# Kernel optimization log

Hardware: AMD Instinct MI355X
Metric: run time of the kernel (lower is better)

## Reference

```python
import jax, jax.numpy as jnp
import numpy as np

N_NODES = 50000
N_EDGES = 160000
D = 512
N_GRAPHS = 64
EPS = 1e-5


def setup_inputs() -> dict:
    key = jax.random.key(0)
    ks = jax.random.split(key, 8)
    node = jax.random.normal(ks[0], (N_NODES, D), dtype=jnp.float32)
    edge_index = jax.random.randint(ks[1], (2, N_EDGES), 0, N_NODES, dtype=jnp.int64)
    edge_attr = jax.random.uniform(ks[2], (N_EDGES,), dtype=jnp.float32)
    batch_ptr = jnp.sort(jax.random.randint(ks[3], (N_NODES,), 0, N_GRAPHS, dtype=jnp.int64))
    W = jax.random.normal(ks[4], (D, D), dtype=jnp.float32) / np.float32(np.sqrt(D))
    b = jnp.zeros((D,), dtype=jnp.float32)
    gn_weight = jnp.ones((D,), dtype=jnp.float32)
    gn_bias = jnp.zeros((D,), dtype=jnp.float32)
    gn_mean_scale = jnp.ones((D,), dtype=jnp.float32)
    return {"node": node, "edge_attr": edge_attr, "W": W, "b": b,
            "gn_weight": gn_weight, "gn_bias": gn_bias, "gn_mean_scale": gn_mean_scale,
            "edge_index": edge_index, "batch_ptr": batch_ptr}


def _gcn_conv(x, edge_index, edge_weight, W, b):
    # x: [N, D]. PyG GCNConv(normalize=True): lin -> add self-loops -> D^-1/2 A D^-1/2 -> + bias
    x = x @ W  # [N, D]
    loop = jnp.arange(N_NODES, dtype=edge_index.dtype)
    row = jnp.concatenate([edge_index[0], loop])  # source
    col = jnp.concatenate([edge_index[1], loop])  # target
    w = jnp.concatenate([edge_weight, jnp.ones((N_NODES,), dtype=x.dtype)])
    deg = jax.ops.segment_sum(w, col, num_segments=N_NODES)  # weighted in-degree incl. self-loop
    dis = jnp.where(deg > 0, jax.lax.rsqrt(deg), 0.0)
    norm = dis[row] * w * dis[col]  # [E+N]
    msgs = x[row] * norm[:, None]  # gather + scale
    out = jax.ops.segment_sum(msgs, col, num_segments=N_NODES)  # scatter-add
    return out + b


def _graph_norm(x, batch, weight, bias, mean_scale):
    # PyG GraphNorm: per-graph mean/var over nodes, learnable mean scale alpha
    ones = jnp.ones((x.shape[0],), dtype=x.dtype)
    count = jax.ops.segment_sum(ones, batch, num_segments=N_GRAPHS)  # [G]
    count = jnp.maximum(count, 1.0)[:, None]
    mean = jax.ops.segment_sum(x, batch, num_segments=N_GRAPHS) / count  # [G, D]
    centered = x - mean[batch] * mean_scale  # [N, D]
    var = jax.ops.segment_sum(centered * centered, batch, num_segments=N_GRAPHS) / count
    inv_std = jax.lax.rsqrt(var + EPS)  # [G, D]
    return weight * centered * inv_std[batch] + bias


def reference(node, edge_attr, W, b, gn_weight, gn_bias, gn_mean_scale, edge_index, batch_ptr):
    conv = _gcn_conv(node, edge_index, edge_attr, W, b)
    h = node + conv  # skip_connection=True
    h = _graph_norm(h, batch_ptr, gn_weight, gn_bias, gn_mean_scale)
    return jax.nn.relu(h)
```

## Files before the change

### kernel.cpp

```cpp
#include <hip/hip_runtime.h>


#define N_NODES 50000
#define PADN    50048
#define N_EDGES 160000
#define DIM 512
#define N_GRAPHS 64
#define EPSV 1e-5f
#define NBLK 196
#define CAP 32

typedef short short8 __attribute__((ext_vector_type(8)));
typedef float floatx4 __attribute__((ext_vector_type(4)));

#define FENCE() do { asm volatile("" ::: "memory"); __builtin_amdgcn_sched_barrier(0); } while (0)

__device__ __forceinline__ unsigned short f2bf(float x) {
    unsigned int u = __float_as_uint(x);
    u += 0x7FFFu + ((u >> 16) & 1u);
    return (unsigned short)(u >> 16);
}
__device__ __forceinline__ float bf2f(unsigned short s) {
    return __uint_as_float(((unsigned int)s) << 16);
}
__device__ __forceinline__ float bflo(int p) {
    return __uint_as_float(((unsigned int)p) << 16);
}
__device__ __forceinline__ float bfhi(int p) {
    return __uint_as_float(((unsigned int)p) & 0xFFFF0000u);
}

__global__ __launch_bounds__(256) void k_setup(const float* __restrict__ node,
                                               const float* __restrict__ W,
                                               short* __restrict__ nodeB,
                                               short* __restrict__ Wt,
                                               float* __restrict__ deg,
                                               float* __restrict__ Sx,
                                               float* __restrict__ Sxx,
                                               float* __restrict__ cntg,
                                               int* __restrict__ cursor) {
    int t = threadIdx.x;
    size_t idx = (size_t)blockIdx.x * 256 + t;
    size_t base = idx * 8;
    int row = (int)(base >> 9);
    int4 o;
    if (row >= N_NODES) {
        o = make_int4(0, 0, 0, 0);
    } else {
        float4 a = *(const float4*)&node[base];
        float4 c = *(const float4*)&node[base + 4];
        o.x = ((unsigned)f2bf(a.y) << 16) | f2bf(a.x);
        o.y = ((unsigned)f2bf(a.w) << 16) | f2bf(a.z);
        o.z = ((unsigned)f2bf(c.y) << 16) | f2bf(c.x);
        o.w = ((unsigned)f2bf(c.w) << 16) | f2bf(c.z);
    }
    *(int4*)&nodeB[base] = o;
    if (blockIdx.x < 1024) {
        int i = blockIdx.x * 256 + t;
        int k = i >> 9, n = i & 511;
        Wt[n * 512 + k] = (short)f2bf(W[i]);
    }
    if (blockIdx.x < NBLK) {
        int i = blockIdx.x * 256 + t;
        if (i < N_NODES) { deg[i] = 1.0f; cursor[i] = 0; }
        if (i < N_GRAPHS * DIM) { Sx[i] = 0.f; Sxx[i] = 0.f; }
        if (i < N_GRAPHS) cntg[i] = 0.f;
    }
}

__global__ __launch_bounds__(256) void k_edges(const int* __restrict__ ei,
                                               const float* __restrict__ ew,
                                               float* __restrict__ deg,
                                               int* __restrict__ cursor,
                                               int* __restrict__ srcs,
                                               float* __restrict__ wts) {
    int e = blockIdx.x * 256 + threadIdx.x;
    if (e >= N_EDGES) return;
    int r = ei[e];
    int c = ei[N_EDGES + e];
    float w = ew[e];
    atomicAdd(&deg[c], w);
    int pos = atomicAdd(&cursor[c], 1);
    if (pos < CAP) {
        srcs[(size_t)c * CAP + pos] = r;
        wts[(size_t)c * CAP + pos] = w;
    }
}

__global__ __launch_bounds__(256) void k_gemm_mfma(const short* __restrict__ Abf,
                                                   const short* __restrict__ Bt,
                                                   short* __restrict__ Cbf) {
    __shared__ short As[2][128 * 64];
    __shared__ short Bs[128 * 64];
    const int tid  = threadIdx.x;
    const int wave = tid >> 6;
    const int lane = tid & 63;
    const int l16  = lane & 15;
    const int quad = lane >> 4;
    const int row0 = blockIdx.y * 128;
    const int col0 = blockIdx.x * 128;
    const int mb = (wave >> 1) * 64;
    const int nb = (wave & 1) * 64;

    floatx4 acc[4][4];
    const floatx4 z = {0.f, 0.f, 0.f, 0.f};
#pragma unroll
    for (int i = 0; i < 4; ++i)
#pragma unroll
        for (int j = 0; j < 4; ++j) acc[i][j] = z;

    const int srow = lane >> 3;
    const int scol = ((lane & 7) ^ srow) * 8;

#define STAGE_A(buf, kk)                                                                  \
    _Pragma("unroll")                                                                     \
    for (int j = 0; j < 4; ++j) {                                                         \
        int seg = wave * 4 + j;                                                           \
        int r = seg * 8 + srow;                                                           \
        __builtin_amdgcn_global_load_lds(                                                 \
            (const __attribute__((address_space(1))) void*)(Abf + (size_t)(row0 + r) * DIM + (kk) + scol), \
            (__attribute__((address_space(3))) void*)(&As[buf][0] + seg * 512 + lane * 8),\
            16, 0, 0);                                                                    \
    }
#define STAGE_B(kk)                                                                       \
    _Pragma("unroll")                                                                     \
    for (int j = 0; j < 4; ++j) {                                                         \
        int seg = wave * 4 + j;                                                           \
        int r = seg * 8 + srow;                                                           \
        __builtin_amdgcn_global_load_lds(                                                 \
            (const __attribute__((address_space(1))) void*)(Bt + (size_t)(col0 + r) * DIM + (kk) + scol),  \
            (__attribute__((address_space(3))) void*)(Bs + seg * 512 + lane * 8),         \
            16, 0, 0);                                                                    \
    }

    STAGE_A(0, 0);
    int cur = 0;
#pragma unroll 1
    for (int t = 0; t < 8; ++t) {
        const int kk = t * 64;
        STAGE_B(kk);
        FENCE();
        if (t < 7) {
            STAGE_A(cur ^ 1, kk + 64);
            FENCE();
            asm volatile("s_waitcnt vmcnt(4)" ::: "memory");
        } else {
            asm volatile("s_waitcnt vmcnt(0)" ::: "memory");
        }
        __builtin_amdgcn_s_barrier();
        FENCE();
#pragma unroll
        for (int kh = 0; kh < 2; ++kh) {
            short8 af[4], bfr[4];
#pragma unroll
            for (int i = 0; i < 4; ++i) {
                int rr = mb + i * 16 + l16;
                int ck = (kh * 4 + quad) ^ (rr & 7);
                af[i] = *(const short8*)&As[cur][rr * 64 + ck * 8];
            }
#pragma unroll
            for (int j = 0; j < 4; ++j) {
                int rb = nb + j * 16 + l16;
                int ck = (kh * 4 + quad) ^ (rb & 7);
                bfr[j] = *(const short8*)&Bs[rb * 64 + ck * 8];
            }
#pragma unroll
            for (int i = 0; i < 4; ++i)
#pragma unroll
                for (int j = 0; j < 4; ++j)
                    acc[i][j] = __builtin_amdgcn_mfma_f32_16x16x32_bf16(bfr[j], af[i], acc[i][j], 0, 0, 0);
        }
        FENCE();
        __builtin_amdgcn_s_barrier();
        cur ^= 1;
    }
#undef STAGE_A
#undef STAGE_B
#pragma unroll
    for (int i = 0; i < 4; ++i) {
        int row = row0 + mb + i * 16 + l16;
#pragma unroll
        for (int j = 0; j < 4; ++j) {
            int col = col0 + nb + j * 16 + quad * 4;
            ushort4 pk;
            pk.x = f2bf(acc[i][j][0]);
            pk.y = f2bf(acc[i][j][1]);
            pk.z = f2bf(acc[i][j][2]);
            pk.w = f2bf(acc[i][j][3]);
            *(ushort4*)&Cbf[(size_t)row * DIM + col] = pk;
        }
    }
}

__global__ __launch_bounds__(256) void k_gather(const int* __restrict__ cursor,
                                                const int* __restrict__ srcs,
                                                const float* __restrict__ wts,
                                                const short* __restrict__ xWb,
                                                short* __restrict__ nodeB,
                                                const float* __restrict__ b,
                                                const float* __restrict__ deg) {
    const int lane = threadIdx.x & 63;
    const int n = __builtin_amdgcn_readfirstlane(blockIdx.x * 4 + (threadIdx.x >> 6));
    const int q = lane * 8;
    const float dn = rsqrtf(deg[n]);
    int cnt = cursor[n];
    if (cnt > CAP) cnt = CAP;
    const size_t ebase = (size_t)n * CAP;

    float a0, a1, a2, a3, a4, a5, a6, a7;
    {
        int4 raw = *(const int4*)&xWb[(size_t)n * DIM + q];
        a0 = dn * bflo(raw.x); a1 = dn * bfhi(raw.x);
        a2 = dn * bflo(raw.y); a3 = dn * bfhi(raw.y);
        a4 = dn * bflo(raw.z); a5 = dn * bfhi(raw.z);
        a6 = dn * bflo(raw.w); a7 = dn * bfhi(raw.w);
    }
    for (int i = 0; i < cnt; ++i) {
        int s = srcs[ebase + i];
        float w = wts[ebase + i] * rsqrtf(deg[s]);
        int4 raw = *(const int4*)&xWb[(size_t)s * DIM + q];
        a0 = fmaf(w, bflo(raw.x), a0); a1 = fmaf(w, bfhi(raw.x), a1);
        a2 = fmaf(w, bflo(raw.y), a2); a3 = fmaf(w, bfhi(raw.y), a3);
        a4 = fmaf(w, bflo(raw.z), a4); a5 = fmaf(w, bfhi(raw.z), a5);
        a6 = fmaf(w, bflo(raw.w), a6); a7 = fmaf(w, bfhi(raw.w), a7);
    }
    int4 nd = *(const int4*)&nodeB[(size_t)n * DIM + q];
    float4 b0 = *(const float4*)&b[q];
    float4 b1 = *(const float4*)&b[q + 4];
    float h0 = bflo(nd.x) + b0.x + dn * a0;
    float h1 = bfhi(nd.x) + b0.y + dn * a1;
    float h2 = bflo(nd.y) + b0.z + dn * a2;
    float h3 = bfhi(nd.y) + b0.w + dn * a3;
    float h4 = bflo(nd.z) + b1.x + dn * a4;
    float h5 = bfhi(nd.z) + b1.y + dn * a5;
    float h6 = bflo(nd.w) + b1.z + dn * a6;
    float h7 = bfhi(nd.w) + b1.w + dn * a7;
    int4 o;
    o.x = ((unsigned)f2bf(h1) << 16) | f2bf(h0);
    o.y = ((unsigned)f2bf(h3) << 16) | f2bf(h2);
    o.z = ((unsigned)f2bf(h5) << 16) | f2bf(h4);
    o.w = ((unsigned)f2bf(h7) << 16) | f2bf(h6);
    *(int4*)&nodeB[(size_t)n * DIM + q] = o;
}

__global__ __launch_bounds__(256) void k_stats(const short* __restrict__ hB,
                                               const int* __restrict__ batch,
                                               float* __restrict__ Sx,
                                               float* __restrict__ Sxx,
                                               float* __restrict__ cntg) {
    const int half = threadIdx.x >> 7;
    const int q = (threadIdx.x & 127) * 4;
    const int lead = (threadIdx.x & 127) == 0;
    const int n0 = blockIdx.x * 128;
    const int g0 = batch[n0];
    int nl = n0 + 127;
    if (nl > N_NODES - 1) nl = N_NODES - 1;
    const int gL = batch[nl];

    if (gL <= g0 + 1) {
        float sxA0 = 0.f, sxA1 = 0.f, sxA2 = 0.f, sxA3 = 0.f;
        float xxA0 = 0.f, xxA1 = 0.f, xxA2 = 0.f, xxA3 = 0.f;
        float sxB0 = 0.f, sxB1 = 0.f, sxB2 = 0.f, sxB3 = 0.f;
        float xxB0 = 0.f, xxB1 = 0.f, xxB2 = 0.f, xxB3 = 0.f;
        float cA = 0.f, cB = 0.f;
#pragma unroll 8
        for (int r = 0; r < 64; ++r) {
            int n = n0 + r * 2 + half;
            int nn = (n < N_NODES) ? n : (N_NODES - 1);
            int g = batch[nn];
            ushort4 hv = *(const ushort4*)&hB[(size_t)n * DIM + q];
            float m = (g == g0) ? 1.f : 0.f;
            float vld = (n < N_NODES) ? 1.f : 0.f;
            float h0 = bf2f(hv.x), h1 = bf2f(hv.y), h2 = bf2f(hv.z), h3 = bf2f(hv.w);
            float a0 = h0 * m, a1 = h1 * m, a2 = h2 * m, a3 = h3 * m;
            sxA0 += a0;            sxA1 += a1;
            sxA2 += a2;            sxA3 += a3;
            xxA0 = fmaf(a0, h0, xxA0); xxA1 = fmaf(a1, h1, xxA1);
            xxA2 = fmaf(a2, h2, xxA2); xxA3 = fmaf(a3, h3, xxA3);
            float b0v = h0 - a0, b1v = h1 - a1, b2v = h2 - a2, b3v = h3 - a3;
            sxB0 += b0v;           sxB1 += b1v;
            sxB2 += b2v;           sxB3 += b3v;
            xxB0 = fmaf(b0v, h0, xxB0); xxB1 = fmaf(b1v, h1, xxB1);
            xxB2 = fmaf(b2v, h2, xxB2); xxB3 = fmaf(b3v, h3, xxB3);
            cA += vld * m;
            cB += vld * (1.f - m);
        }
        atomicAdd(&Sx[g0 * DIM + q + 0], sxA0);
        atomicAdd(&Sx[g0 * DIM + q + 1], sxA1);
        atomicAdd(&Sx[g0 * DIM + q + 2], sxA2);
        atomicAdd(&Sx[g0 * DIM + q + 3], sxA3);
        atomicAdd(&Sxx[g0 * DIM + q + 0], xxA0);
        atomicAdd(&Sxx[g0 * DIM + q + 1], xxA1);
        atomicAdd(&Sxx[g0 * DIM + q + 2], xxA2);
        atomicAdd(&Sxx[g0 * DIM + q + 3], xxA3);
        if (lead) atomicAdd(&cntg[g0], cA);
        if (gL != g0) {
            atomicAdd(&Sx[gL * DIM + q + 0], sxB0);
            atomicAdd(&Sx[gL * DIM + q + 1], sxB1);
            atomicAdd(&Sx[gL * DIM + q + 2], sxB2);
            atomicAdd(&Sx[gL * DIM + q + 3], sxB3);
            atomicAdd(&Sxx[gL * DIM + q + 0], xxB0);
            atomicAdd(&Sxx[gL * DIM + q + 1], xxB1);
            atomicAdd(&Sxx[gL * DIM + q + 2], xxB2);
            atomicAdd(&Sxx[gL * DIM + q + 3], xxB3);
            if (lead) atomicAdd(&cntg[gL], cB);
        }
    } else {
        for (int r = 0; r < 64; ++r) {
            int n = n0 + r * 2 + half;
            if (n >= N_NODES) break;
            int g = batch[n];
            ushort4 hv = *(const ushort4*)&hB[(size_t)n * DIM + q];
            float h0 = bf2f(hv.x), h1 = bf2f(hv.y), h2 = bf2f(hv.z), h3 = bf2f(hv.w);
            atomicAdd(&Sx[g * DIM + q + 0], h0);
            atomicAdd(&Sx[g * DIM + q + 1], h1);
            atomicAdd(&Sx[g * DIM + q + 2], h2);
            atomicAdd(&Sx[g * DIM + q + 3], h3);
            atomicAdd(&Sxx[g * DIM + q + 0], h0 * h0);
            atomicAdd(&Sxx[g * DIM + q + 1], h1 * h1);
            atomicAdd(&Sxx[g * DIM + q + 2], h2 * h2);
            atomicAdd(&Sxx[g * DIM + q + 3], h3 * h3);
            if (lead) atomicAdd(&cntg[g], 1.f);
        }
    }
}

__global__ __launch_bounds__(256) void k_norm(const short* __restrict__ hB,
                                              const int* __restrict__ batch,
                                              const float* __restrict__ Sx,
                                              const float* __restrict__ Sxx,
                                              const float* __restrict__ cntg,
                                              const float* __restrict__ alpha,
                                              const float* __restrict__ gw,
                                              const float* __restrict__ gb,
                                              float* __restrict__ out) {
    size_t idx = (size_t)blockIdx.x * 256 + threadIdx.x;
    int n = (int)(idx >> 7);
    int q = ((int)idx & 127) * 4;
    if (n >= N_NODES) return;
    int g = batch[n];
    float c = fmaxf(cntg[g], 1.0f);
    float rc = __builtin_amdgcn_rcpf(c);
    float4 sx = *(const float4*)&Sx[(size_t)g * DIM + q];
    float4 xx = *(const float4*)&Sxx[(size_t)g * DIM + q];
    float4 al = *(const float4*)&alpha[q];
    float4 w4 = *(const float4*)&gw[q];
    float4 b4 = *(const float4*)&gb[q];
    ushort4 hv = *(const ushort4*)&hB[(size_t)n * DIM + q];
    float m0 = sx.x * rc, m1 = sx.y * rc, m2 = sx.z * rc, m3 = sx.w * rc;
    float ma0 = m0 * al.x, ma1 = m1 * al.y, ma2 = m2 * al.z, ma3 = m3 * al.w;
    float iv0 = rsqrtf(xx.x * rc - 2.f * m0 * ma0 + ma0 * ma0 + EPSV);
    float iv1 = rsqrtf(xx.y * rc - 2.f * m1 * ma1 + ma1 * ma1 + EPSV);
    float iv2 = rsqrtf(xx.z * rc - 2.f * m2 * ma2 + ma2 * ma2 + EPSV);
    float iv3 = rsqrtf(xx.w * rc - 2.f * m3 * ma3 + ma3 * ma3 + EPSV);
    float4 r;
    r.x = fmaxf(0.f, (bf2f(hv.x) - ma0) * iv0 * w4.x + b4.x);
    r.y = fmaxf(0.f, (bf2f(hv.y) - ma1) * iv1 * w4.y + b4.y);
    r.z = fmaxf(0.f, (bf2f(hv.z) - ma2) * iv2 * w4.z + b4.z);
    r.w = fmaxf(0.f, (bf2f(hv.w) - ma3) * iv3 * w4.w + b4.w);
    *(float4*)&out[(size_t)n * DIM + q] = r;
}

extern "C" void kernel_launch(void* const* d_in, const int* in_sizes, int n_in,
                              void* d_out, int out_size, void* d_ws, size_t ws_size,
                              hipStream_t stream) {
    const float* node  = (const float*)d_in[0];
    const float* eattr = (const float*)d_in[1];
    const float* W     = (const float*)d_in[2];
    const float* b     = (const float*)d_in[3];
    const float* gw    = (const float*)d_in[4];
    const float* gb    = (const float*)d_in[5];
    const float* alpha = (const float*)d_in[6];
    const int*   ei    = (const int*)d_in[7];
    const int*   batch = (const int*)d_in[8];
    float* out = (float*)d_out;

    short* nodeB = (short*)d_ws;
    short* xWb   = nodeB + (size_t)PADN * DIM;
    short* Wt    = xWb + (size_t)PADN * DIM;
    float* deg   = (float*)(Wt + DIM * DIM);
    float* Sx    = deg + N_NODES;
    float* Sxx   = Sx + N_GRAPHS * DIM;
    float* cntg  = Sxx + N_GRAPHS * DIM;
    float* wts   = cntg + 64;
    int* cursor  = (int*)(wts + (size_t)N_NODES * CAP);
    int* srcs    = cursor + N_NODES;

    k_setup<<<PADN * DIM / 8 / 256, 256, 0, stream>>>(node, W, nodeB, Wt,
                                                      deg, Sx, Sxx, cntg, cursor);
    k_edges<<<(N_EDGES + 255) / 256, 256, 0, stream>>>(ei, eattr, deg, cursor, srcs, wts);
    dim3 ggrid(4, PADN / 128);
    k_gemm_mfma<<<ggrid, 256, 0, stream>>>(nodeB, Wt, xWb);
    k_gather<<<N_NODES / 4, 256, 0, stream>>>(cursor, srcs, wts, xWb, nodeB, b, deg);
    k_stats<<<(N_NODES + 127) / 128, 256, 0, stream>>>(nodeB, batch, Sx, Sxx, cntg);
    k_norm<<<25000, 256, 0, stream>>>(nodeB, batch, Sx, Sxx, cntg, alpha, gw, gb, out);
}
```

Baseline: 356.7 us.

## Fuse fp32-to-bf16 node conversion into GEMM A-tile loading and merge setup kernels

Drops the separate pass that converted the whole node matrix to bf16. The GEMM now loads fp32 A tiles into registers, packs them with v_cvt_pk_bf16_f32 and writes them to LDS. The skip connection in the gather kernel reads fp32 node directly. Zeroing moves to a small dedicated kernel, and the edge bucketing merges with the W transpose, so deg becomes 1+degsum. The stats kernel also switches to 64-node blocks for more parallelism. The cost is register-staged A loads in place of direct global-to-LDS loads, with twice the A bytes read inside the GEMM.

```diff
diff --git a/kernel.cpp b/kernel.cpp
--- a/kernel.cpp
+++ b/kernel.cpp
@@ -7,8 +7,9 @@
 #define DIM 512
 #define N_GRAPHS 64
 #define EPSV 1e-5f
-#define NBLK 196
 #define CAP 32
+
+#define ZWORDS (2 * N_NODES + 2 * N_GRAPHS * DIM + N_GRAPHS)
 
 typedef short short8 __attribute__((ext_vector_type(8)));
 typedef float floatx4 __attribute__((ext_vector_type(4)));
@@ -29,65 +30,49 @@
 __device__ __forceinline__ float bfhi(int p) {
     return __uint_as_float(((unsigned int)p) & 0xFFFF0000u);
 }
-
-__global__ __launch_bounds__(256) void k_setup(const float* __restrict__ node,
-                                               const float* __restrict__ W,
-                                               short* __restrict__ nodeB,
-                                               short* __restrict__ Wt,
-                                               float* __restrict__ deg,
-                                               float* __restrict__ Sx,
-                                               float* __restrict__ Sxx,
-                                               float* __restrict__ cntg,
-                                               int* __restrict__ cursor) {
+__device__ __forceinline__ int pkbf(float lo, float hi) {
+    int r;
+    asm("v_cvt_pk_bf16_f32 %0, %1, %2" : "=v"(r) : "v"(lo), "v"(hi));
+    return r;
+}
+
+__global__ __launch_bounds__(256) void k_zero(int* __restrict__ z) {
+    int i = (blockIdx.x * 256 + threadIdx.x) * 4;
+    if (i < ZWORDS) {
+        int4 zz = make_int4(0, 0, 0, 0);
+        *(int4*)&z[i] = zz;
+    }
+}
+
+__global__ __launch_bounds__(256) void k_prep(const float* __restrict__ W,
+                                              short* __restrict__ Wt,
+                                              const int* __restrict__ ei,
+                                              const float* __restrict__ ew,
+                                              float* __restrict__ degsum,
+                                              int* __restrict__ cursor,
+                                              int* __restrict__ srcs,
+                                              float* __restrict__ wts) {
     int t = threadIdx.x;
-    size_t idx = (size_t)blockIdx.x * 256 + t;
-    size_t base = idx * 8;
-    int row = (int)(base >> 9);
-    int4 o;
-    if (row >= N_NODES) {
-        o = make_int4(0, 0, 0, 0);
-    } else {
-        float4 a = *(const float4*)&node[base];
-        float4 c = *(const float4*)&node[base + 4];
-        o.x = ((unsigned)f2bf(a.y) << 16) | f2bf(a.x);
-        o.y = ((unsigned)f2bf(a.w) << 16) | f2bf(a.z);
-        o.z = ((unsigned)f2bf(c.y) << 16) | f2bf(c.x);
-        o.w = ((unsigned)f2bf(c.w) << 16) | f2bf(c.z);
-    }
-    *(int4*)&nodeB[base] = o;
-    if (blockIdx.x < 1024) {
+    {
         int i = blockIdx.x * 256 + t;
         int k = i >> 9, n = i & 511;
         Wt[n * 512 + k] = (short)f2bf(W[i]);
     }
-    if (blockIdx.x < NBLK) {
-        int i = blockIdx.x * 256 + t;
-        if (i < N_NODES) { deg[i] = 1.0f; cursor[i] = 0; }
-        if (i < N_GRAPHS * DIM) { Sx[i] = 0.f; Sxx[i] = 0.f; }
-        if (i < N_GRAPHS) cntg[i] = 0.f;
-    }
-}
-
-__global__ __launch_bounds__(256) void k_edges(const int* __restrict__ ei,
-                                               const float* __restrict__ ew,
-                                               float* __restrict__ deg,
-                                               int* __restrict__ cursor,
-                                               int* __restrict__ srcs,
-                                               float* __restrict__ wts) {
-    int e = blockIdx.x * 256 + threadIdx.x;
-    if (e >= N_EDGES) return;
-    int r = ei[e];
-    int c = ei[N_EDGES + e];
-    float w = ew[e];
-    atomicAdd(&deg[c], w);
-    int pos = atomicAdd(&cursor[c], 1);
-    if (pos < CAP) {
-        srcs[(size_t)c * CAP + pos] = r;
-        wts[(size_t)c * CAP + pos] = w;
-    }
-}
-
-__global__ __launch_bounds__(256) void k_gemm_mfma(const short* __restrict__ Abf,
+    if (blockIdx.x < 625) {
+        int e = blockIdx.x * 256 + t;
+        int r = ei[e];
+        int c = ei[N_EDGES + e];
+        float w = ew[e];
+        atomicAdd(&degsum[c], w);
+        int pos = atomicAdd(&cursor[c], 1);
+        if (pos < CAP) {
+            srcs[(size_t)c * CAP + pos] = r;
+            wts[(size_t)c * CAP + pos] = w;
+        }
+    }
+}
+
+__global__ __launch_bounds__(256) void k_gemm_mfma(const float* __restrict__ Af,
                                                    const short* __restrict__ Bt,
                                                    short* __restrict__ Cbf) {
     __shared__ short As[2][128 * 64];
@@ -112,15 +97,26 @@
     const int srow = lane >> 3;
     const int scol = ((lane & 7) ^ srow) * 8;
 
-#define STAGE_A(buf, kk)                                                                  \
+    float4 av0[4], av1[4];
+
+#define LOAD_A_REGS(kk)                                                                   \
     _Pragma("unroll")                                                                     \
     for (int j = 0; j < 4; ++j) {                                                         \
-        int seg = wave * 4 + j;                                                           \
-        int r = seg * 8 + srow;                                                           \
-        __builtin_amdgcn_global_load_lds(                                                 \
-            (const __attribute__((address_space(1))) void*)(Abf + (size_t)(row0 + r) * DIM + (kk) + scol), \
-            (__attribute__((address_space(3))) void*)(&As[buf][0] + seg * 512 + lane * 8),\
-            16, 0, 0);                                                                    \
+        int grow = row0 + wave * 32 + j * 8 + srow;                                       \
+        if (grow > N_NODES - 1) grow = N_NODES - 1;         \
+        const float* src = Af + (size_t)grow * DIM + (kk) + scol;                         \
+        av0[j] = *(const float4*)src;                                                     \
+        av1[j] = *(const float4*)(src + 4);                                               \
+    }
+#define WRITE_A_LDS(buf)                                                                  \
+    _Pragma("unroll")                                                                     \
+    for (int j = 0; j < 4; ++j) {                                                         \
+        int4 o;                                                                           \
+        o.x = pkbf(av0[j].x, av0[j].y);                                                   \
+        o.y = pkbf(av0[j].z, av0[j].w);                                                   \
+        o.z = pkbf(av1[j].x, av1[j].y);                                                   \
+        o.w = pkbf(av1[j].z, av1[j].w);                                                   \
+        *(int4*)&As[buf][(wave * 4 + j) * 512 + lane * 8] = o;                            \
     }
 #define STAGE_B(kk)                                                                       \
     _Pragma("unroll")                                                                     \
@@ -133,19 +129,21 @@
             16, 0, 0);                                                                    \
     }
 
-    STAGE_A(0, 0);
+    LOAD_A_REGS(0);
     int cur = 0;
 #pragma unroll 1
     for (int t = 0; t < 8; ++t) {
         const int kk = t * 64;
         STAGE_B(kk);
         FENCE();
+        WRITE_A_LDS(cur);
+        FENCE();
         if (t < 7) {
-            STAGE_A(cur ^ 1, kk + 64);
+            LOAD_A_REGS(kk + 64);
             FENCE();
-            asm volatile("s_waitcnt vmcnt(4)" ::: "memory");
+            asm volatile("s_waitcnt vmcnt(8) lgkmcnt(0)" ::: "memory");
         } else {
-            asm volatile("s_waitcnt vmcnt(0)" ::: "memory");
+            asm volatile("s_waitcnt vmcnt(0) lgkmcnt(0)" ::: "memory");
         }
         __builtin_amdgcn_s_barrier();
         FENCE();
@@ -174,7 +172,8 @@
         __builtin_amdgcn_s_barrier();
         cur ^= 1;
     }
-#undef STAGE_A
+#undef LOAD_A_REGS
+#undef WRITE_A_LDS
 #undef STAGE_B
 #pragma unroll
     for (int i = 0; i < 4; ++i) {
@@ -196,13 +195,19 @@
                                                 const int* __restrict__ srcs,
                                                 const float* __restrict__ wts,
                                                 const short* __restrict__ xWb,
-                                                short* __restrict__ nodeB,
+                                                const float* __restrict__ node,
+                                                short* __restrict__ hbuf,
                                                 const float* __restrict__ b,
-                                                const float* __restrict__ deg) {
+                                                const float* __restrict__ degsum) {
     const int lane = threadIdx.x & 63;
     const int n = __builtin_amdgcn_readfirstlane(blockIdx.x * 4 + (threadIdx.x >> 6));
     const int q = lane * 8;
-    const float dn = rsqrtf(deg[n]);
+    if (n >= N_NODES) {
+        int4 zz = make_int4(0, 0, 0, 0);
+        *(int4*)&hbuf[(size_t)n * DIM + q] = zz;
+        return;
+    }
+    const float dn = rsqrtf(1.0f + degsum[n]);
     int cnt = cursor[n];
     if (cnt > CAP) cnt = CAP;
     const size_t ebase = (size_t)n * CAP;
@@ -217,30 +222,31 @@
     }
     for (int i = 0; i < cnt; ++i) {
         int s = srcs[ebase + i];
-        float w = wts[ebase + i] * rsqrtf(deg[s]);
+        float w = wts[ebase + i] * rsqrtf(1.0f + degsum[s]);
         int4 raw = *(const int4*)&xWb[(size_t)s * DIM + q];
         a0 = fmaf(w, bflo(raw.x), a0); a1 = fmaf(w, bfhi(raw.x), a1);
         a2 = fmaf(w, bflo(raw.y), a2); a3 = fmaf(w, bfhi(raw.y), a3);
         a4 = fmaf(w, bflo(raw.z), a4); a5 = fmaf(w, bfhi(raw.z), a5);
         a6 = fmaf(w, bflo(raw.w), a6); a7 = fmaf(w, bfhi(raw.w), a7);
     }
-    int4 nd = *(const int4*)&nodeB[(size_t)n * DIM + q];
+    float4 x0 = *(const float4*)&node[(size_t)n * DIM + q];
+    float4 x1 = *(const float4*)&node[(size_t)n * DIM + q + 4];
     float4 b0 = *(const float4*)&b[q];
     float4 b1 = *(const float4*)&b[q + 4];
-    float h0 = bflo(nd.x) + b0.x + dn * a0;
-    float h1 = bfhi(nd.x) + b0.y + dn * a1;
-    float h2 = bflo(nd.y) + b0.z + dn * a2;
-    float h3 = bfhi(nd.y) + b0.w + dn * a3;
-    float h4 = bflo(nd.z) + b1.x + dn * a4;
-    float h5 = bfhi(nd.z) + b1.y + dn * a5;
-    float h6 = bflo(nd.w) + b1.z + dn * a6;
-    float h7 = bfhi(nd.w) + b1.w + dn * a7;
+    float h0 = x0.x + b0.x + dn * a0;
+    float h1 = x0.y + b0.y + dn * a1;
+    float h2 = x0.z + b0.z + dn * a2;
+    float h3 = x0.w + b0.w + dn * a3;
+    float h4 = x1.x + b1.x + dn * a4;
+    float h5 = x1.y + b1.y + dn * a5;
+    float h6 = x1.z + b1.z + dn * a6;
+    float h7 = x1.w + b1.w + dn * a7;
     int4 o;
     o.x = ((unsigned)f2bf(h1) << 16) | f2bf(h0);
     o.y = ((unsigned)f2bf(h3) << 16) | f2bf(h2);
     o.z = ((unsigned)f2bf(h5) << 16) | f2bf(h4);
     o.w = ((unsigned)f2bf(h7) << 16) | f2bf(h6);
-    *(int4*)&nodeB[(size_t)n * DIM + q] = o;
+    *(int4*)&hbuf[(size_t)n * DIM + q] = o;
 }
 
 __global__ __launch_bounds__(256) void k_stats(const short* __restrict__ hB,
@@ -251,9 +257,9 @@
     const int half = threadIdx.x >> 7;
     const int q = (threadIdx.x & 127) * 4;
     const int lead = (threadIdx.x & 127) == 0;
-    const int n0 = blockIdx.x * 128;
+    const int n0 = blockIdx.x * 64;
     const int g0 = batch[n0];
-    int nl = n0 + 127;
+    int nl = n0 + 63;
     if (nl > N_NODES - 1) nl = N_NODES - 1;
     const int gL = batch[nl];
 
@@ -264,7 +270,7 @@
         float xxB0 = 0.f, xxB1 = 0.f, xxB2 = 0.f, xxB3 = 0.f;
         float cA = 0.f, cB = 0.f;
 #pragma unroll 8
-        for (int r = 0; r < 64; ++r) {
+        for (int r = 0; r < 32; ++r) {
             int n = n0 + r * 2 + half;
             int nn = (n < N_NODES) ? n : (N_NODES - 1);
             int g = batch[nn];
@@ -306,7 +312,7 @@
             if (lead) atomicAdd(&cntg[gL], cB);
         }
     } else {
-        for (int r = 0; r < 64; ++r) {
+        for (int r = 0; r < 32; ++r) {
             int n = n0 + r * 2 + half;
             if (n >= N_NODES) break;
             int g = batch[n];
@@ -375,23 +381,22 @@
     const int*   batch = (const int*)d_in[8];
     float* out = (float*)d_out;
 
-    short* nodeB = (short*)d_ws;
-    short* xWb   = nodeB + (size_t)PADN * DIM;
-    short* Wt    = xWb + (size_t)PADN * DIM;
-    float* deg   = (float*)(Wt + DIM * DIM);
-    float* Sx    = deg + N_NODES;
-    float* Sxx   = Sx + N_GRAPHS * DIM;
-    float* cntg  = Sxx + N_GRAPHS * DIM;
-    float* wts   = cntg + 64;
-    int* cursor  = (int*)(wts + (size_t)N_NODES * CAP);
-    int* srcs    = cursor + N_NODES;
-
-    k_setup<<<PADN * DIM / 8 / 256, 256, 0, stream>>>(node, W, nodeB, Wt,
-                                                      deg, Sx, Sxx, cntg, cursor);
-    k_edges<<<(N_EDGES + 255) / 256, 256, 0, stream>>>(ei, eattr, deg, cursor, srcs, wts);
+    short* hbuf   = (short*)d_ws;
+    short* xWb    = hbuf + (size_t)PADN * DIM;
+    short* Wt     = xWb + (size_t)PADN * DIM;
+    float* degsum = (float*)(Wt + DIM * DIM);
+    int*   cursor = (int*)(degsum + N_NODES);
+    float* Sx     = (float*)(cursor + N_NODES);
+    float* Sxx    = Sx + N_GRAPHS * DIM;
+    float* cntg   = Sxx + N_GRAPHS * DIM;
+    float* wts    = cntg + N_GRAPHS;
+    int*   srcs   = (int*)(wts + (size_t)N_NODES * CAP);
+
+    k_zero<<<(ZWORDS / 4 + 255) / 256, 256, 0, stream>>>((int*)degsum);
+    k_prep<<<1024, 256, 0, stream>>>(W, Wt, ei, eattr, degsum, cursor, srcs, wts);
     dim3 ggrid(4, PADN / 128);
-    k_gemm_mfma<<<ggrid, 256, 0, stream>>>(nodeB, Wt, xWb);
-    k_gather<<<N_NODES / 4, 256, 0, stream>>>(cursor, srcs, wts, xWb, nodeB, b, deg);
-    k_stats<<<(N_NODES + 127) / 128, 256, 0, stream>>>(nodeB, batch, Sx, Sxx, cntg);
-    k_norm<<<25000, 256, 0, stream>>>(nodeB, batch, Sx, Sxx, cntg, alpha, gw, gb, out);
-}
+    k_gemm_mfma<<<ggrid, 256, 0, stream>>>(node, Wt, xWb);
+    k_gather<<<PADN / 4, 256, 0, stream>>>(cursor, srcs, wts, xWb, node, hbuf, b, degsum);
+    k_stats<<<(N_NODES + 63) / 64, 256, 0, stream>>>(hbuf, batch, Sx, Sxx, cntg);
+    k_norm<<<25000, 256, 0, stream>>>(hbuf, batch, Sx, Sxx, cntg, alpha, gw, gb, out);
+}
```

New measurement: 375.7 us. 1.05x slower.
